# Performance work log

Hardware: AMD Instinct MI355X
Metric: run time of the kernel (lower is better)

The kernel has to match this reference:

```python
import jax, jax.numpy as jnp
from jax import lax
import numpy as np

B, T, IN, H, L = 64, 512, 256, 512, 2


def setup_inputs() -> dict:
    key = jax.random.key(0)
    k = jax.random.split(key, 5)
    s_w = 1.0 / np.sqrt(IN)
    s_u = 1.0 / np.sqrt(H)
    return {
        "x": jax.random.normal(k[0], (B, T, IN), dtype=jnp.float32),
        "W": jax.random.uniform(k[1], (3 * H, IN), dtype=jnp.float32, minval=-s_w, maxval=s_w),
        "b_W": jax.random.uniform(k[2], (3 * H,), dtype=jnp.float32, minval=-s_w, maxval=s_w),
        "U": jax.random.uniform(k[3], (3 * H, H), dtype=jnp.float32, minval=-s_u, maxval=s_u),
        "b_U": jax.random.uniform(k[4], (3 * H,), dtype=jnp.float32, minval=-s_u, maxval=s_u),
        "num_layers": L,
    }


def _cell(xt, h, W, b_W, U, b_U):
    # xt: [B, IN], h: [B, H]
    xg = xt @ W.T + b_W          # [B, 3H]
    hg = h @ U.T + b_U           # [B, 3H]
    xr, xu, xn = jnp.split(xg, 3, axis=1)
    hr, hu, hn = jnp.split(hg, 3, axis=1)
    r = jax.nn.sigmoid(xr + hr)
    u = jax.nn.sigmoid(xu + hu)
    n = jnp.tanh(xn + r * hn)
    return u * h + (1.0 - u) * n


def reference(x, W, b_W, U, b_U, num_layers):
    b, t, _ = x.shape
    hdim = U.shape[1]

    def step(h, xt):
        hs = []
        for _ in range(num_layers):  # shared cell reapplied to same xt
            h = _cell(xt, h, W, b_W, U, b_U)
            hs.append(h)
        return h, jnp.stack(hs)      # [L, B, H]

    h0 = jnp.zeros((b, hdim), x.dtype)
    _, hs = lax.scan(step, h0, jnp.swapaxes(x, 0, 1))  # [T, L, B, H]
    return hs.reshape(t * num_layers, b, hdim)
```

## Files before the change

### kernel.cpp

```cpp
#include <hip/hip_runtime.h>
#include <stdint.h>

#define BB   64
#define TT   512
#define KIN  256
#define HH   512
#define JGN  16
#define BGN  4
#define NJ2  32
#define NB   16
#define XPAD 260

typedef short bf16x8 __attribute__((ext_vector_type(8)));
typedef float f32x4  __attribute__((ext_vector_type(4)));

union U16x8 { unsigned short s[8]; bf16x8 v; };
union FU    { float f; unsigned u; };

__device__ __forceinline__ unsigned short f2bf(float f){
  FU v; v.f = f;
  unsigned r = v.u + 0x7fffu + ((v.u >> 16) & 1u);
  return (unsigned short)(r >> 16);
}
__device__ __forceinline__ float bf2f(unsigned short s){
  FU v; v.u = ((unsigned)s) << 16; return v.f;
}
__device__ __forceinline__ bf16x8 cvt8(const float* p){
  float4 a = ((const float4*)p)[0];
  float4 b = ((const float4*)p)[1];
  float f[8] = {a.x,a.y,a.z,a.w,b.x,b.y,b.z,b.w};
  U16x8 h;
  #pragma unroll
  for(int i=0;i<8;i++) h.s[i] = f2bf(f[i]);
  return h.v;
}
__device__ __forceinline__ void split8(const float* p, bf16x8& hi, bf16x8& lo){
  float4 a = ((const float4*)p)[0];
  float4 b = ((const float4*)p)[1];
  float f[8] = {a.x,a.y,a.z,a.w,b.x,b.y,b.z,b.w};
  U16x8 h,l;
  #pragma unroll
  for(int i=0;i<8;i++){
    unsigned short hb = f2bf(f[i]);
    l.s[i] = f2bf(f[i] - bf2f(hb));
    h.s[i] = hb;
  }
  hi = h.v; lo = l.v;
}
__device__ __forceinline__ void unpackg(uint4 A, uint4 B, bf16x8& hi, bf16x8& lo){
  unsigned wv[8] = {A.x,A.y,A.z,A.w,B.x,B.y,B.z,B.w};
  U16x8 h,l;
  #pragma unroll
  for(int j=0;j<8;j++){
    h.s[j] = (unsigned short)(wv[j] >> 16);
    l.s[j] = (unsigned short)(wv[j] & 0xffffu);
  }
  hi = h.v; lo = l.v;
}

#define MFMA __builtin_amdgcn_mfma_f32_16x16x32_bf16

#define LD4W(Q0,Q1,Q2,Q3, BASE) \
  asm volatile( \
    "global_load_dwordx4 %0, %4, off sc1\n\t" \
    "global_load_dwordx4 %1, %4, off offset:16 sc1\n\t" \
    "global_load_dwordx4 %2, %4, off offset:128 sc1\n\t" \
    "global_load_dwordx4 %3, %4, off offset:144 sc1\n\t" \
    "s_waitcnt vmcnt(0)" \
    : "=&v"(Q0),"=&v"(Q1),"=&v"(Q2),"=&v"(Q3) \
    : "v"(BASE) : "memory")

__global__ __launch_bounds__(512, 1) void gru_scan(
    const float* __restrict__ x,  const float* __restrict__ Wm,
    const float* __restrict__ bW, const float* __restrict__ Um,
    const float* __restrict__ bU, float* __restrict__ out,
    unsigned* __restrict__ hbuf,  unsigned* __restrict__ flags)
{
  __shared__ f32x4 red [8][6][64];
  __shared__ f32x4 red2[8][6][64];
  __shared__ float xlds[NB][XPAD];

  const int tid  = threadIdx.x;
  const int u    = tid >> 6;
  const int lane = tid & 63;
  const int col  = lane & 15;
  const int lg   = lane >> 4;
  const int bid  = blockIdx.x;
  const int bg   = bid >> 4;
  const int jg   = bid & 15;
  const int j0   = jg * NJ2;
  const int b0g  = bg * NB;

  bf16x8 BU[6][2], BW[6];
  #pragma unroll
  for(int nt=0; nt<6; nt++){
    int rl   = nt*16 + col;
    int g    = rl >> 5, jj = rl & 31;
    int grow = g*HH + j0 + jj;
    #pragma unroll
    for(int ks=0; ks<2; ks++){
      int kb = u*64 + ks*32 + lg*8;
      BU[nt][ks] = cvt8(Um + (size_t)grow*HH + kb);
    }
    BW[nt] = cvt8(Wm + (size_t)grow*KIN + u*32 + lg*8);
  }

  float bsr, bsu, bwn, bun;
  {
    int jl = (u & 1)*16 + col;
    int r0 = j0 + jl;
    bsr = bW[r0]        + bU[r0];
    bsu = bW[HH + r0]   + bU[HH + r0];
    bwn = bW[2*HH + r0];
    bun = bU[2*HH + r0];
  }

  float hreg[4] = {0.f,0.f,0.f,0.f};

  auto stage_x = [&](int tt){
    #pragma unroll
    for(int i=0; i<2; i++){
      int bl = u*2 + i;
      const float* gp = x + ((size_t)(b0g + bl)*TT + tt)*KIN + lane*4;
      __builtin_amdgcn_global_load_lds(
        (const __attribute__((address_space(1))) unsigned*)(const void*)gp,
        (__attribute__((address_space(3))) unsigned*)(void*)&xlds[bl][0],
        16, 0, 0);
    }
  };

  auto xg_partials = [&](){
    f32x4 Cx[6];
    #pragma unroll
    for(int nt=0;nt<6;nt++) Cx[nt]=(f32x4){0,0,0,0};
    bf16x8 ah, al;
    split8(&xlds[col][u*32 + lg*8], ah, al);
    #pragma unroll
    for(int nt=0; nt<6; nt++){
      Cx[nt] = MFMA(ah, BW[nt], Cx[nt], 0,0,0);
      Cx[nt] = MFMA(al, BW[nt], Cx[nt], 0,0,0);
    }
    #pragma unroll
    for(int nt=0;nt<6;nt++) red2[u][nt][lane] = Cx[nt];
  };

  auto xg_reduce = [&](f32x4 (&xg)[3]){
    #pragma unroll
    for(int gi=0; gi<3; gi++){
      int nt = gi*2 + u;
      f32x4 s = red2[0][nt][lane];
      #pragma unroll
      for(int pw=1; pw<8; pw++) s += red2[pw][nt][lane];
      xg[gi] = s;
    }
  };

  auto run_cell = [&](const unsigned* hb, unsigned* hw, int cell,
                      const f32x4 (&xgf)[3], float (&on)[4]){
    const void* a0 = (const char*)(hb + (size_t)(b0g + col)*HH + u*64 + lg*8);
    uint4 q0,q1,q2,q3;
    LD4W(q0,q1,q2,q3, a0);
    __builtin_amdgcn_sched_barrier(0);

    f32x4 Ch[6];
    #pragma unroll
    for(int nt=0;nt<6;nt++) Ch[nt]=(f32x4){0,0,0,0};
    {
      bf16x8 ah, al;
      unpackg(q0,q1,ah,al);
      #pragma unroll
      for(int nt=0; nt<6; nt++){
        Ch[nt] = MFMA(ah, BU[nt][0], Ch[nt], 0,0,0);
        Ch[nt] = MFMA(al, BU[nt][0], Ch[nt], 0,0,0);
      }
      unpackg(q2,q3,ah,al);
      #pragma unroll
      for(int nt=0; nt<6; nt++){
        Ch[nt] = MFMA(ah, BU[nt][1], Ch[nt], 0,0,0);
        Ch[nt] = MFMA(al, BU[nt][1], Ch[nt], 0,0,0);
      }
    }
    #pragma unroll
    for(int nt=0;nt<6;nt++) red[u][nt][lane] = Ch[nt];
    __syncthreads();

    if(u < 2){
      f32x4 hg[3];
      #pragma unroll
      for(int gi=0; gi<3; gi++){
        int nt = gi*2 + u;
        f32x4 s = red[0][nt][lane];
        #pragma unroll
        for(int pw=1; pw<8; pw++) s += red[pw][nt][lane];
        hg[gi] = s;
      }
      #pragma unroll
      for(int r=0;r<4;r++){
        float pr = xgf[0][r] + hg[0][r] + bsr;
        float pu = xgf[1][r] + hg[1][r] + bsu;
        float rg = __builtin_amdgcn_rcpf(1.f + __expf(-pr));
        float ug = __builtin_amdgcn_rcpf(1.f + __expf(-pu));
        float hn = hg[2][r] + bun;
        float z  = xgf[2][r] + bwn + rg*hn;
        z = fminf(fmaxf(z, -15.f), 15.f);
        float e  = __expf(2.f*z);
        float nn = (e - 1.f) * __builtin_amdgcn_rcpf(e + 1.f);
        float hnew = ug*hreg[r] + (1.f - ug)*nn;
        hreg[r] = hnew;
        on[r]   = hnew;
        unsigned short h16 = f2bf(hnew);
        unsigned short l16 = f2bf(hnew - bf2f(h16));
        __hip_atomic_store(&hw[(size_t)(b0g + lg*4 + r)*HH + j0 + u*16 + col],
                           ((unsigned)h16 << 16) | (unsigned)l16,
                           __ATOMIC_RELAXED, __HIP_MEMORY_SCOPE_AGENT);
      }
    }
    __syncthreads();
    if(tid == 0)
      __hip_atomic_store(&flags[bid], (unsigned)cell + 1u,
                         __ATOMIC_RELAXED, __HIP_MEMORY_SCOPE_AGENT);
  };

  auto poll = [&](int tgt){
    const unsigned* fp = flags + bg*16;
    while(true){
      unsigned f = __hip_atomic_load(&fp[lane & 15], __ATOMIC_RELAXED,
                                     __HIP_MEMORY_SCOPE_AGENT);
      if(__all((int)(f >= (unsigned)tgt))) break;
      __builtin_amdgcn_s_sleep(1);
    }
    __builtin_amdgcn_sched_barrier(0);
    asm volatile("" ::: "memory");
  };

  auto out_store = [&](int cell, const float (&on)[4]){
    if(u < 2){
      #pragma unroll
      for(int r=0;r<4;r++)
        out[((size_t)cell*BB + b0g + lg*4 + r)*HH + j0 + u*16 + col] = on[r];
    }
  };

  unsigned* hb0 = hbuf;
  unsigned* hb1 = hbuf + (size_t)BB*HH;

  f32x4 xgf[3] = {(f32x4){0,0,0,0},(f32x4){0,0,0,0},(f32x4){0,0,0,0}};
  f32x4 xgn[3] = {(f32x4){0,0,0,0},(f32x4){0,0,0,0},(f32x4){0,0,0,0}};
  float on0[4] = {0,0,0,0}, on1[4] = {0,0,0,0};

  stage_x(0);
  __syncthreads();
  xg_partials();
  __syncthreads();
  if(u < 2) xg_reduce(xgf);

  for(int t=0; t<TT; t++){
    run_cell(hb0, hb1, 2*t, xgf, on0);
    if(t+1 < TT) stage_x(t+1);
    out_store(2*t, on0);
    poll(2*t + 1);
    run_cell(hb1, hb0, 2*t + 1, xgf, on1);
    if(t+1 < TT){
      xg_partials();
      __syncthreads();
      if(u < 2) xg_reduce(xgn);
    }
    out_store(2*t + 1, on1);
    if(t+1 < TT) poll(2*t + 2);
    xgf[0] = xgn[0]; xgf[1] = xgn[1]; xgf[2] = xgn[2];
  }
}

extern "C" void kernel_launch(void* const* d_in, const int* in_sizes, int n_in,
                              void* d_out, int out_size, void* d_ws, size_t ws_size,
                              hipStream_t stream) {
  const float* x  = (const float*)d_in[0];
  const float* Wm = (const float*)d_in[1];
  const float* bW = (const float*)d_in[2];
  const float* Um = (const float*)d_in[3];
  const float* bU = (const float*)d_in[4];
  float* out = (float*)d_out;

  unsigned* hbuf  = (unsigned*)d_ws;
  unsigned* flags = (unsigned*)((char*)d_ws + 2*BB*HH*sizeof(unsigned));
  (void)hipMemsetAsync(d_ws, 0, 2*BB*HH*sizeof(unsigned) + 256, stream);

  gru_scan<<<BGN*JGN, 512, 0, stream>>>(x, Wm, bW, Um, bU, out, hbuf, flags);
}
```

Before: 3.474 ms.

## Poll only producer flags per wave and move input-projection MFMAs earlier

New measurement: 3.445 ms. About the same (-0.8%).

```diff
diff --git a/kernel.cpp b/kernel.cpp
--- a/kernel.cpp
+++ b/kernel.cpp
@@ -98,19 +98,16 @@
     int g    = rl >> 5, jj = rl & 31;
     int grow = g*HH + j0 + jj;
     #pragma unroll
-    for(int ks=0; ks<2; ks++){
-      int kb = u*64 + ks*32 + lg*8;
-      BU[nt][ks] = cvt8(Um + (size_t)grow*HH + kb);
-    }
+    for(int ks=0; ks<2; ks++)
+      BU[nt][ks] = cvt8(Um + (size_t)grow*HH + u*64 + ks*32 + lg*8);
     BW[nt] = cvt8(Wm + (size_t)grow*KIN + u*32 + lg*8);
   }
 
   float bsr, bsu, bwn, bun;
   {
-    int jl = (u & 1)*16 + col;
-    int r0 = j0 + jl;
-    bsr = bW[r0]        + bU[r0];
-    bsu = bW[HH + r0]   + bU[HH + r0];
+    int r0 = j0 + (u & 1)*16 + col;
+    bsr = bW[r0]      + bU[r0];
+    bsu = bW[HH + r0] + bU[HH + r0];
     bwn = bW[2*HH + r0];
     bun = bU[2*HH + r0];
   }
@@ -129,39 +126,23 @@
     }
   };
 
-  auto xg_partials = [&](){
-    f32x4 Cx[6];
-    #pragma unroll
-    for(int nt=0;nt<6;nt++) Cx[nt]=(f32x4){0,0,0,0};
-    bf16x8 ah, al;
-    split8(&xlds[col][u*32 + lg*8], ah, al);
-    #pragma unroll
-    for(int nt=0; nt<6; nt++){
-      Cx[nt] = MFMA(ah, BW[nt], Cx[nt], 0,0,0);
-      Cx[nt] = MFMA(al, BW[nt], Cx[nt], 0,0,0);
-    }
-    #pragma unroll
-    for(int nt=0;nt<6;nt++) red2[u][nt][lane] = Cx[nt];
-  };
-
-  auto xg_reduce = [&](f32x4 (&xg)[3]){
-    #pragma unroll
-    for(int gi=0; gi<3; gi++){
-      int nt = gi*2 + u;
-      f32x4 s = red2[0][nt][lane];
-      #pragma unroll
-      for(int pw=1; pw<8; pw++) s += red2[pw][nt][lane];
-      xg[gi] = s;
-    }
-  };
-
-  auto run_cell = [&](const unsigned* hb, unsigned* hw, int cell,
-                      const f32x4 (&xgf)[3], float (&on)[4]){
+  auto pollw = [&](int tgt){
+    const unsigned* fp = flags + bg*JGN + 2*u;
+    while(true){
+      unsigned f = __hip_atomic_load(&fp[lane & 1], __ATOMIC_RELAXED,
+                                     __HIP_MEMORY_SCOPE_AGENT);
+      if(__all((int)(f >= (unsigned)tgt))) break;
+      __builtin_amdgcn_s_sleep(1);
+    }
+    __builtin_amdgcn_sched_barrier(0);
+    asm volatile("" ::: "memory");
+  };
+
+  auto h_mfma = [&](const unsigned* hb){
     const void* a0 = (const char*)(hb + (size_t)(b0g + col)*HH + u*64 + lg*8);
     uint4 q0,q1,q2,q3;
     LD4W(q0,q1,q2,q3, a0);
     __builtin_amdgcn_sched_barrier(0);
-
     f32x4 Ch[6];
     #pragma unroll
     for(int nt=0;nt<6;nt++) Ch[nt]=(f32x4){0,0,0,0};
@@ -182,55 +163,64 @@
     }
     #pragma unroll
     for(int nt=0;nt<6;nt++) red[u][nt][lane] = Ch[nt];
-    __syncthreads();
-
-    if(u < 2){
-      f32x4 hg[3];
-      #pragma unroll
-      for(int gi=0; gi<3; gi++){
-        int nt = gi*2 + u;
-        f32x4 s = red[0][nt][lane];
-        #pragma unroll
-        for(int pw=1; pw<8; pw++) s += red[pw][nt][lane];
-        hg[gi] = s;
-      }
-      #pragma unroll
-      for(int r=0;r<4;r++){
-        float pr = xgf[0][r] + hg[0][r] + bsr;
-        float pu = xgf[1][r] + hg[1][r] + bsu;
-        float rg = __builtin_amdgcn_rcpf(1.f + __expf(-pr));
-        float ug = __builtin_amdgcn_rcpf(1.f + __expf(-pu));
-        float hn = hg[2][r] + bun;
-        float z  = xgf[2][r] + bwn + rg*hn;
-        z = fminf(fmaxf(z, -15.f), 15.f);
-        float e  = __expf(2.f*z);
-        float nn = (e - 1.f) * __builtin_amdgcn_rcpf(e + 1.f);
-        float hnew = ug*hreg[r] + (1.f - ug)*nn;
-        hreg[r] = hnew;
-        on[r]   = hnew;
-        unsigned short h16 = f2bf(hnew);
-        unsigned short l16 = f2bf(hnew - bf2f(h16));
-        __hip_atomic_store(&hw[(size_t)(b0g + lg*4 + r)*HH + j0 + u*16 + col],
-                           ((unsigned)h16 << 16) | (unsigned)l16,
-                           __ATOMIC_RELAXED, __HIP_MEMORY_SCOPE_AGENT);
-      }
-    }
-    __syncthreads();
-    if(tid == 0)
-      __hip_atomic_store(&flags[bid], (unsigned)cell + 1u,
+  };
+
+  auto xg_partials = [&](){
+    f32x4 Cx[6];
+    #pragma unroll
+    for(int nt=0;nt<6;nt++) Cx[nt]=(f32x4){0,0,0,0};
+    bf16x8 ah, al;
+    split8(&xlds[col][u*32 + lg*8], ah, al);
+    #pragma unroll
+    for(int nt=0; nt<6; nt++){
+      Cx[nt] = MFMA(ah, BW[nt], Cx[nt], 0,0,0);
+      Cx[nt] = MFMA(al, BW[nt], Cx[nt], 0,0,0);
+    }
+    #pragma unroll
+    for(int nt=0;nt<6;nt++) red2[u][nt][lane] = Cx[nt];
+  };
+
+  auto xg_reduce = [&](f32x4 (&xg)[3]){
+    #pragma unroll
+    for(int gi=0; gi<3; gi++){
+      int nt = gi*2 + u;
+      f32x4 s = red2[0][nt][lane];
+      #pragma unroll
+      for(int pw=1; pw<8; pw++) s += red2[pw][nt][lane];
+      xg[gi] = s;
+    }
+  };
+
+  auto gates = [&](unsigned* hw, const f32x4 (&xgf)[3], float (&on)[4]){
+    f32x4 hg[3];
+    #pragma unroll
+    for(int gi=0; gi<3; gi++){
+      int nt = gi*2 + u;
+      f32x4 s = red[0][nt][lane];
+      #pragma unroll
+      for(int pw=1; pw<8; pw++) s += red[pw][nt][lane];
+      hg[gi] = s;
+    }
+    #pragma unroll
+    for(int r=0;r<4;r++){
+      float pr = xgf[0][r] + hg[0][r] + bsr;
+      float pu = xgf[1][r] + hg[1][r] + bsu;
+      float rg = __builtin_amdgcn_rcpf(1.f + __expf(-pr));
+      float ug = __builtin_amdgcn_rcpf(1.f + __expf(-pu));
+      float hn = hg[2][r] + bun;
+      float z  = xgf[2][r] + bwn + rg*hn;
+      z = fminf(fmaxf(z, -15.f), 15.f);
+      float e  = __expf(2.f*z);
+      float nn = (e - 1.f) * __builtin_amdgcn_rcpf(e + 1.f);
+      float hnew = ug*hreg[r] + (1.f - ug)*nn;
+      hreg[r] = hnew;
+      on[r]   = hnew;
+      unsigned short h16 = f2bf(hnew);
+      unsigned short l16 = f2bf(hnew - bf2f(h16));
+      __hip_atomic_store(&hw[(size_t)(b0g + lg*4 + r)*HH + j0 + u*16 + col],
+                         ((unsigned)h16 << 16) | (unsigned)l16,
                          __ATOMIC_RELAXED, __HIP_MEMORY_SCOPE_AGENT);
-  };
-
-  auto poll = [&](int tgt){
-    const unsigned* fp = flags + bg*16;
-    while(true){
-      unsigned f = __hip_atomic_load(&fp[lane & 15], __ATOMIC_RELAXED,
-                                     __HIP_MEMORY_SCOPE_AGENT);
-      if(__all((int)(f >= (unsigned)tgt))) break;
-      __builtin_amdgcn_s_sleep(1);
-    }
-    __builtin_amdgcn_sched_barrier(0);
-    asm volatile("" ::: "memory");
+    }
   };
 
   auto out_store = [&](int cell, const float (&on)[4]){
@@ -253,20 +243,33 @@
   xg_partials();
   __syncthreads();
   if(u < 2) xg_reduce(xgf);
+  stage_x(1);
+  __syncthreads();
 
   for(int t=0; t<TT; t++){
-    run_cell(hb0, hb1, 2*t, xgf, on0);
-    if(t+1 < TT) stage_x(t+1);
+    pollw(2*t);
+    h_mfma(hb0);
+    if(t+1 < TT) xg_partials();
+    __syncthreads();
+    if(u < 2) gates(hb1, xgf, on0);
+    __syncthreads();
+    if(tid == 0)
+      __hip_atomic_store(&flags[bid & 63], (unsigned)(2*t) + 1u,
+                         __ATOMIC_RELAXED, __HIP_MEMORY_SCOPE_AGENT);
+    if(u < 2 && t+1 < TT) xg_reduce(xgn);
     out_store(2*t, on0);
-    poll(2*t + 1);
-    run_cell(hb1, hb0, 2*t + 1, xgf, on1);
-    if(t+1 < TT){
-      xg_partials();
-      __syncthreads();
-      if(u < 2) xg_reduce(xgn);
-    }
+
+    if(t+2 < TT) stage_x(t+2);
+    pollw(2*t + 1);
+    h_mfma(hb1);
+    __syncthreads();
+    if(u < 2) gates(hb0, xgf, on1);
+    __syncthreads();
+    if(tid == 0)
+      __hip_atomic_store(&flags[bid & 63], (unsigned)(2*t) + 2u,
+                         __ATOMIC_RELAXED, __HIP_MEMORY_SCOPE_AGENT);
     out_store(2*t + 1, on1);
-    if(t+1 < TT) poll(2*t + 2);
+
     xgf[0] = xgn[0]; xgf[1] = xgn[1]; xgf[2] = xgn[2];
   }
 }
```
